# Kernel optimization log

Hardware: AMD Instinct MI355X
Metric: run time of the kernel (lower is better)

Reference implementation:

```python
import jax, jax.numpy as jnp
import numpy as np

HID = 4096
NH = 32
NKV = 8
HD = 128
KV_OUT = NKV * HD  # 1024
B, S = 1, 2048
SCALE = 64.0
THETA = 500000.0


def fwht(x):
    """Normalized fast Walsh-Hadamard transform over last dim (power of 2).
    Matches matmul_hadU_cuda for the had=None, K=1 case."""
    *lead, n = x.shape
    x = x.reshape(-1, n)
    h = 1
    while h < n:  # log2(n) static iterations
        x = x.reshape(-1, n // (2 * h), 2, h)
        a, b = x[:, :, 0, :], x[:, :, 1, :]
        x = jnp.stack([a + b, a - b], axis=2).reshape(-1, n)
        h *= 2
    return (x * (1.0 / np.sqrt(n))).reshape(*lead, n)


def rope_cos_sin(position_ids, dim=HD, theta=THETA):
    inv_freq = 1.0 / (theta ** (jnp.arange(0, dim, 2, dtype=jnp.float32) / dim))
    freqs = position_ids.astype(jnp.float32)[..., None] * inv_freq  # [B,S,HD/2]
    emb = jnp.concatenate([freqs, freqs], axis=-1)  # [B,S,HD]
    return jnp.cos(emb), jnp.sin(emb)


def rotate_half(x):
    h = x.shape[-1] // 2
    return jnp.concatenate([-x[..., h:], x[..., :h]], axis=-1)


def setup_inputs() -> dict:
    key = jax.random.key(0)
    ks = jax.random.split(key, 10)
    return {
        "hidden_states": jax.random.normal(ks[0], (B, S, HID), jnp.float32),
        "position_ids": jnp.arange(S, dtype=jnp.int32)[None, :],
        "SU_qkv": jnp.sign(jax.random.normal(ks[1], (HID,), jnp.float32)),
        "SU_o": jnp.sign(jax.random.normal(ks[2], (HID,), jnp.float32)),
        "Wscale_qkv": jax.random.uniform(ks[3], (HID + 2 * KV_OUT,), jnp.float32, 0.5, 1.5),
        "Wscale_o": jax.random.uniform(ks[4], (HID,), jnp.float32, 0.5, 1.5),
        "Wq": 0.02 * jax.random.normal(ks[5], (HID, HID), jnp.float32),
        "Wk": 0.02 * jax.random.normal(ks[6], (KV_OUT, HID), jnp.float32),
        "Wv": 0.02 * jax.random.normal(ks[7], (KV_OUT, HID), jnp.float32),
        "Wo": 0.02 * jax.random.normal(ks[8], (HID, HID), jnp.float32),
    }


def reference(hidden_states, position_ids, SU_qkv, SU_o, Wscale_qkv, Wscale_o, Wq, Wk, Wv, Wo):
    b, s, n = hidden_states.shape
    # --- compute_qkv: incoherence rotation + quantized-linear math ---
    x = fwht(hidden_states * SU_qkv) / SCALE  # [B,S,HID]
    q = (x @ Wq.T) * Wscale_qkv[:HID] * SCALE
    k = (x @ Wk.T) * Wscale_qkv[HID:HID + KV_OUT] * SCALE
    v = (x @ Wv.T) * Wscale_qkv[HID + KV_OUT:] * SCALE
    q = q.reshape(b, s, NH, HD).transpose(0, 2, 1, 3)   # [B,NH,S,HD]
    k = k.reshape(b, s, NKV, HD).transpose(0, 2, 1, 3)  # [B,NKV,S,HD]
    v = v.reshape(b, s, NKV, HD).transpose(0, 2, 1, 3)
    # --- RoPE ---
    cos, sin = rope_cos_sin(position_ids)
    cos, sin = cos[:, None], sin[:, None]  # [B,1,S,HD]
    q = q * cos + rotate_half(q) * sin
    k = k * cos + rotate_half(k) * sin
    # --- GQA repeat + causal SDPA ---
    rep = NH // NKV
    k = jnp.repeat(k, rep, axis=1)
    v = jnp.repeat(v, rep, axis=1)
    scores = jnp.einsum('bhqd,bhkd->bhqk', q, k) / np.sqrt(HD)
    causal = jnp.tril(jnp.ones((s, s), dtype=bool))
    scores = jnp.where(causal, scores, -1e30)
    attn = jax.nn.softmax(scores, axis=-1)
    out = jnp.einsum('bhqk,bhkd->bhqd', attn, v)
    out = out.transpose(0, 2, 1, 3).reshape(b, s, NH * HD)  # [B,S,HID]
    # --- compute_o ---
    y = fwht(out * SU_o) / SCALE
    y = (y @ Wo.T) * Wscale_o * SCALE
    return y
```

## Files before the change

### kernel.cpp

```cpp
#include <hip/hip_runtime.h>
#include <hip/hip_bf16.h>
#include <math.h>

#define S_LEN 2048
#define HID   4096
#define NQKV  6144
#define NHEAD 32
#define NKVH  8
#define HDIM  128

typedef __attribute__((ext_vector_type(8))) short short8;
typedef __attribute__((ext_vector_type(4))) float f32x4;

__device__ __forceinline__ unsigned short f2bf(float f) {
    union { float f; unsigned u; } v; v.f = f;
    unsigned r = v.u + 0x7fffu + ((v.u >> 16) & 1u);
    return (unsigned short)(r >> 16);
}
__device__ __forceinline__ float bf2f(unsigned short b) {
    union { unsigned u; float f; } v; v.u = ((unsigned)b) << 16;
    return v.f;
}
__device__ __forceinline__ unsigned cvt_pk_bf16(float lo, float hi) {
    unsigned r;
    asm("v_cvt_pk_bf16_f32 %0, %1, %2" : "=v"(r) : "v"(lo), "v"(hi));
    return r;
}

__global__ __launch_bounds__(256)
void cvt4_kernel(const float* __restrict__ Wq, const float* __restrict__ Wk,
                 const float* __restrict__ Wv, const float* __restrict__ Wo,
                 unsigned short* __restrict__ Wcat, unsigned short* __restrict__ Wob) {
    const int NQ = 4194304, NK = 1048576, NV = 1048576, NO = 4194304;
    int i = blockIdx.x * 256 + threadIdx.x;
    const int stride = gridDim.x * 256;
    for (; i < NQ + NK + NV + NO; i += stride) {
        const float* src; unsigned short* dst; int j;
        if (i < NQ)                { src = Wq; dst = Wcat;            j = i; }
        else if (i < NQ + NK)      { src = Wk; dst = Wcat + 16777216; j = i - NQ; }
        else if (i < NQ + NK + NV) { src = Wv; dst = Wcat + 20971520; j = i - NQ - NK; }
        else                       { src = Wo; dst = Wob;             j = i - NQ - NK - NV; }
        float4 v = *(const float4*)(src + (size_t)j * 4);
        ushort4 o;
        o.x = f2bf(v.x); o.y = f2bf(v.y); o.z = f2bf(v.z); o.w = f2bf(v.w);
        *(ushort4*)(dst + (size_t)j * 4) = o;
    }
}

__global__ __launch_bounds__(256)
void fwht_kernel(const float* __restrict__ in, const float* __restrict__ su,
                 unsigned short* __restrict__ out) {
    __shared__ float buf[HID];
    const float* src = in + (size_t)blockIdx.x * HID;
    for (int i = threadIdx.x; i < HID; i += 256) buf[i] = src[i] * su[i];
    __syncthreads();
    int lg = 0;
    for (int h = 1; h < HID; h <<= 1, ++lg) {
        for (int p = threadIdx.x; p < HID / 2; p += 256) {
            int j  = p & (h - 1);
            int i0 = ((p >> lg) << (lg + 1)) | j;
            int i1 = i0 + h;
            float a = buf[i0], b = buf[i1];
            buf[i0] = a + b;
            buf[i1] = a - b;
        }
        __syncthreads();
    }
    unsigned short* dst = out + (size_t)blockIdx.x * HID;
    const float norm = 1.0f / 4096.0f;
    for (int i = threadIdx.x; i < HID; i += 256) dst[i] = f2bf(buf[i] * norm);
}

__global__ __launch_bounds__(256)
void fwht_merge(const unsigned short* __restrict__ O1, const float* __restrict__ ML,
                const float* __restrict__ su, unsigned short* __restrict__ out) {
    __shared__ float buf[HID];
    __shared__ float w1s[NHEAD], w2s[NHEAD];
    const int q = blockIdx.x;
    if (threadIdx.x < NHEAD) {
        const float2* mlp = (const float2*)ML;
        float2 a = mlp[((size_t)q) * NHEAD + threadIdx.x];
        float2 b = mlp[((size_t)(S_LEN + q)) * NHEAD + threadIdx.x];
        float M = fmaxf(a.x, b.x);
        float e1 = exp2f(a.x - M), e2 = exp2f(b.x - M);
        float L = e1 * a.y + e2 * b.y;
        w1s[threadIdx.x] = e1 / L;
        w2s[threadIdx.x] = e2 / L;
    }
    __syncthreads();
    const unsigned short* r1 = O1 + (size_t)q * HID;
    const unsigned short* r2 = O1 + (size_t)(S_LEN + q) * HID;
    for (int i = threadIdx.x; i < HID; i += 256) {
        int hd = i >> 7;
        buf[i] = (bf2f(r1[i]) * w1s[hd] + bf2f(r2[i]) * w2s[hd]) * su[i];
    }
    __syncthreads();
    int lg = 0;
    for (int h = 1; h < HID; h <<= 1, ++lg) {
        for (int p = threadIdx.x; p < HID / 2; p += 256) {
            int j  = p & (h - 1);
            int i0 = ((p >> lg) << (lg + 1)) | j;
            int i1 = i0 + h;
            float a = buf[i0], b = buf[i1];
            buf[i0] = a + b;
            buf[i1] = a - b;
        }
        __syncthreads();
    }
    unsigned short* dst = out + (size_t)q * HID;
    const float norm = 1.0f / 4096.0f;
    for (int i = threadIdx.x; i < HID; i += 256) dst[i] = f2bf(buf[i] * norm);
}

__global__ __launch_bounds__(256)
void gemm_bt(const unsigned short* __restrict__ A, const unsigned short* __restrict__ B,
             const float* __restrict__ scale, float* __restrict__ C,
             int M, int N, int K) {
    __shared__ __attribute__((aligned(16))) unsigned short As[2][128 * 32];
    __shared__ __attribute__((aligned(16))) unsigned short Bs[2][128 * 32];
    const int bn = blockIdx.x, bm = blockIdx.y;
    const int tid = threadIdx.x;
    const int wv = tid >> 6, lane = tid & 63;
    const int wr = wv >> 1, wc = wv & 1;
    const int lr = lane & 15, lgp = lane >> 4;

    f32x4 acc[4][4] = {};

    auto stage = [&](int buf, int kt) {
        for (int c = wv; c < 8; c += 4) {
            int o = c * 512 + lane * 8;
            int row = o >> 5, col = o & 31;
            const unsigned short* ga = A + (size_t)(bm * 128 + row) * K + kt * 32 + col;
            __builtin_amdgcn_global_load_lds((const __attribute__((address_space(1))) void*)ga,
                (__attribute__((address_space(3))) void*)&As[buf][c * 512], 16, 0, 0);
            const unsigned short* gb = B + (size_t)(bn * 128 + row) * K + kt * 32 + col;
            __builtin_amdgcn_global_load_lds((const __attribute__((address_space(1))) void*)gb,
                (__attribute__((address_space(3))) void*)&Bs[buf][c * 512], 16, 0, 0);
        }
    };

    const int nt = K >> 5;
    stage(0, 0);
    __syncthreads();
    int cur = 0;
    for (int kt = 0; kt < nt; ++kt) {
        if (kt + 1 < nt) stage(cur ^ 1, kt + 1);
        const int ko = lgp * 8;
        short8 af[4], bfr[4];
#pragma unroll
        for (int m2 = 0; m2 < 4; ++m2)
            af[m2] = *(const short8*)&As[cur][(wr * 64 + m2 * 16 + lr) * 32 + ko];
#pragma unroll
        for (int n2 = 0; n2 < 4; ++n2)
            bfr[n2] = *(const short8*)&Bs[cur][(wc * 64 + n2 * 16 + lr) * 32 + ko];
#pragma unroll
        for (int m2 = 0; m2 < 4; ++m2)
#pragma unroll
            for (int n2 = 0; n2 < 4; ++n2)
                acc[m2][n2] = __builtin_amdgcn_mfma_f32_16x16x32_bf16(af[m2], bfr[n2], acc[m2][n2], 0, 0, 0);
        __syncthreads();
        cur ^= 1;
    }

#pragma unroll
    for (int n2 = 0; n2 < 4; ++n2) {
        int gn = bn * 128 + wc * 64 + n2 * 16 + lr;
        float sc = scale[gn] * 64.0f;
#pragma unroll
        for (int m2 = 0; m2 < 4; ++m2) {
            int gm0 = bm * 128 + wr * 64 + m2 * 16 + lgp * 4;
#pragma unroll
            for (int i = 0; i < 4; ++i)
                C[(size_t)(gm0 + i) * N + gn] = acc[m2][n2][i] * sc;
        }
    }
}

__global__ __launch_bounds__(256)
void rope_kernel(const float* __restrict__ qkv, const int* __restrict__ pos,
                 unsigned short* __restrict__ Qb, unsigned short* __restrict__ Kb,
                 unsigned short* __restrict__ Vb) {
    __shared__ float invf_t[64];
    if (threadIdx.x < 64)
        invf_t[threadIdx.x] = exp2f((float)threadIdx.x * -0.29580576f);
    __syncthreads();
    const int s = blockIdx.x;
    const float p = (float)pos[s];
    const float* row = qkv + (size_t)s * NQKV;
    const float qs = 0.12751793f;
    for (int idx = threadIdx.x; idx < NQKV; idx += 256) {
        float v = row[idx];
        if (idx < HID + NKVH * HDIM) {
            int base = (idx < HID) ? 0 : HID;
            int rel = idx - base;
            int h = rel >> 7, d = rel & 127;
            float ang = p * invf_t[d & 63];
            float sn, cs;
            sincosf(ang, &sn, &cs);
            float other = (d < 64) ? -row[base + h * 128 + d + 64]
                                   :  row[base + h * 128 + d - 64];
            float r = v * cs + other * sn;
            if (idx < HID) Qb[((size_t)h * S_LEN + s) * HDIM + d] = f2bf(r * qs);
            else           Kb[((size_t)h * S_LEN + s) * HDIM + d] = f2bf(r);
        } else {
            int rel = idx - (HID + NKVH * HDIM);
            int h = rel >> 7, d = rel & 127;
            Vb[((size_t)h * S_LEN + s) * HDIM + d] = f2bf(v);
        }
    }
}

__global__ __launch_bounds__(256)
void attn_kernel(const unsigned short* __restrict__ Q, const unsigned short* __restrict__ K,
                 const unsigned short* __restrict__ V, unsigned short* __restrict__ Opart,
                 float* __restrict__ ML) {
    const int hf = blockIdx.y;
    const int hd = blockIdx.z;
    const int kvh = hd >> 2;
    const int tid = threadIdx.x, wv = tid >> 6, lane = tid & 63;
    const int lr = lane & 15, lgp = lane >> 4;

    __shared__ __attribute__((aligned(16))) unsigned short Ks[2][64 * 128];
    __shared__ __attribute__((aligned(16))) unsigned short Vt[128 * 64];

    int koff[4];
#pragma unroll
    for (int j = 0; j < 4; ++j) {
        int a = (wv * 4 + j) * 512 + lane * 8;
        koff[j] = a ^ (((a >> 7) & 7) << 3);
    }
    const int vpos = ((lane >> 2) & 3) * 16 + (lane >> 4) * 4 + (lane & 3);
    const unsigned short* Kg = K + (size_t)kvh * S_LEN * HDIM;
    const unsigned short* Vg = V + (size_t)kvh * S_LEN * HDIM;

    auto stageK = [&](int buf, int kb) {
        const unsigned short* kg = Kg + (size_t)kb * 64 * HDIM;
#pragma unroll
        for (int j = 0; j < 4; ++j) {
            __builtin_amdgcn_global_load_lds(
                (const __attribute__((address_space(1))) void*)(kg + koff[j]),
                (__attribute__((address_space(3))) void*)&Ks[buf][(wv * 4 + j) * 512], 16, 0, 0);
        }
    };

#pragma unroll 1
    for (int rep = 0; rep < 2; ++rep) {
        const int qt = rep ? (31 - (int)blockIdx.x) : (int)blockIdx.x;
        const int qg = qt * 64 + wv * 16 + lr;
        const int n = qt + 1, mid = (n + 1) >> 1;
        const int s = hf ? mid : 0, e = hf ? n : mid;

        __syncthreads();

        short8 aq[4];
        {
            const unsigned short* qp = Q + ((size_t)hd * S_LEN + qg) * HDIM + lgp * 8;
#pragma unroll
            for (int kk = 0; kk < 4; ++kk) aq[kk] = *(const short8*)(qp + kk * 32);
        }

        f32x4 oacc[8] = {};
        float m_i = -3.0e38f, l_i = 0.f;

        short8 vcur[4];
        if (s < e) {
            stageK(s & 1, s);
            const unsigned short* vp = Vg + (size_t)s * 64 * HDIM + lane * HDIM + wv * 32;
#pragma unroll
            for (int r2 = 0; r2 < 4; ++r2) vcur[r2] = *(const short8*)(vp + r2 * 8);
        }

#pragma unroll 1
        for (int kb = s; kb < e; ++kb) {
            const int cur = kb & 1;
            __syncthreads();

            if (kb + 1 < e) stageK(cur ^ 1, kb + 1);
#pragma unroll
            for (int r2 = 0; r2 < 4; ++r2) {
#pragma unroll
                for (int en = 0; en < 8; ++en) {
                    int d = wv * 32 + r2 * 8 + en;
                    Vt[(d * 64 + vpos) ^ ((d & 7) << 3)] = ((const unsigned short*)&vcur[r2])[en];
                }
            }
            if (kb + 1 < e) {
                const unsigned short* vp = Vg + (size_t)(kb + 1) * 64 * HDIM + lane * HDIM + wv * 32;
#pragma unroll
                for (int r2 = 0; r2 < 4; ++r2) vcur[r2] = *(const short8*)(vp + r2 * 8);
            }

            __builtin_amdgcn_s_setprio(1);
            f32x4 sc[4];
#pragma unroll
            for (int nt2 = 0; nt2 < 4; ++nt2) {
                f32x4 a = {};
                const int krow = nt2 * 16 + lr;
                const int swz = (krow & 7) << 3;
#pragma unroll
                for (int kk = 0; kk < 4; ++kk) {
                    short8 ak = *(const short8*)&Ks[cur][(krow * 128 + kk * 32 + lgp * 8) ^ swz];
                    a = __builtin_amdgcn_mfma_f32_16x16x32_bf16(ak, aq[kk], a, 0, 0, 0);
                }
                sc[nt2] = a;
            }
            __builtin_amdgcn_s_setprio(0);

            if (kb == qt) {
#pragma unroll
                for (int nt2 = 0; nt2 < 4; ++nt2)
#pragma unroll
                    for (int i = 0; i < 4; ++i) {
                        int kvg = kb * 64 + nt2 * 16 + 4 * lgp + i;
                        if (kvg > qg) sc[nt2][i] = -1.0e30f;
                    }
            }

            float vmax = fmaxf(fmaxf(fmaxf(sc[0][0], sc[0][1]), fmaxf(sc[0][2], sc[0][3])),
                               fmaxf(fmaxf(sc[1][0], sc[1][1]), fmaxf(sc[1][2], sc[1][3])));
            vmax = fmaxf(vmax, fmaxf(fmaxf(fmaxf(sc[2][0], sc[2][1]), fmaxf(sc[2][2], sc[2][3])),
                                     fmaxf(fmaxf(sc[3][0], sc[3][1]), fmaxf(sc[3][2], sc[3][3]))));
            vmax = fmaxf(vmax, __shfl_xor(vmax, 16));
            vmax = fmaxf(vmax, __shfl_xor(vmax, 32));

            if (!__all(vmax <= m_i + 11.0f)) {
                float mn = fmaxf(m_i, vmax);
                float fe = __builtin_amdgcn_exp2f(m_i - mn);
                m_i = mn;
                l_i *= fe;
                float feb[4];
#pragma unroll
                for (int i2 = 0; i2 < 4; ++i2) feb[i2] = __shfl(fe, 4 * lgp + i2);
#pragma unroll
                for (int t = 0; t < 8; ++t)
#pragma unroll
                    for (int i2 = 0; i2 < 4; ++i2) oacc[t][i2] *= feb[i2];
            }

            float rs = 0.f;
#pragma unroll
            for (int nt2 = 0; nt2 < 4; ++nt2)
#pragma unroll
                for (int i = 0; i < 4; ++i) {
                    float pv = __builtin_amdgcn_exp2f(sc[nt2][i] - m_i);
                    sc[nt2][i] = pv;
                    rs += pv;
                }
            rs += __shfl_xor(rs, 16);
            rs += __shfl_xor(rs, 32);
            l_i += rs;

            union { unsigned u[4]; short8 sv; } a0, a1;
            a0.u[0] = cvt_pk_bf16(sc[0][0], sc[0][1]);
            a0.u[1] = cvt_pk_bf16(sc[0][2], sc[0][3]);
            a0.u[2] = cvt_pk_bf16(sc[1][0], sc[1][1]);
            a0.u[3] = cvt_pk_bf16(sc[1][2], sc[1][3]);
            a1.u[0] = cvt_pk_bf16(sc[2][0], sc[2][1]);
            a1.u[1] = cvt_pk_bf16(sc[2][2], sc[2][3]);
            a1.u[2] = cvt_pk_bf16(sc[3][0], sc[3][1]);
            a1.u[3] = cvt_pk_bf16(sc[3][2], sc[3][3]);

            asm volatile("s_waitcnt lgkmcnt(0)" ::: "memory");
            __builtin_amdgcn_sched_barrier(0);
            __builtin_amdgcn_s_barrier();

            __builtin_amdgcn_s_setprio(1);
#pragma unroll
            for (int t = 0; t < 8; ++t) {
                const int d = t * 16 + lr;
                const int swz = (d & 7) << 3;
                const int dbase = d * 64 + lgp * 16;
                short8 bv0 = *(const short8*)&Vt[(dbase) ^ swz];
                short8 bv1 = *(const short8*)&Vt[(dbase + 8) ^ swz];
                oacc[t] = __builtin_amdgcn_mfma_f32_16x16x32_bf16(a0.sv, bv0, oacc[t], 0, 0, 0);
                oacc[t] = __builtin_amdgcn_mfma_f32_16x16x32_bf16(a1.sv, bv1, oacc[t], 0, 0, 0);
            }
            __builtin_amdgcn_s_setprio(0);
        }

        unsigned short* op = Opart + ((size_t)hf * S_LEN + qt * 64 + wv * 16 + 4 * lgp) * HID
                           + hd * HDIM + lr;
#pragma unroll
        for (int t = 0; t < 8; ++t)
#pragma unroll
            for (int i2 = 0; i2 < 4; ++i2)
                op[(size_t)i2 * HID + t * 16] = f2bf(oacc[t][i2]);
        if (lgp == 0) {
            float2* mlp = (float2*)ML;
            mlp[((size_t)hf * S_LEN + qt * 64 + wv * 16 + lr) * NHEAD + hd] =
                make_float2(m_i, l_i);
        }
    }
}

extern "C" void kernel_launch(void* const* d_in, const int* in_sizes, int n_in,
                              void* d_out, int out_size, void* d_ws, size_t ws_size,
                              hipStream_t stream) {
    const float* hidden = (const float*)d_in[0];
    const int*   pos    = (const int*)d_in[1];
    const float* su_qkv = (const float*)d_in[2];
    const float* su_o   = (const float*)d_in[3];
    const float* ws_qkv = (const float*)d_in[4];
    const float* ws_o   = (const float*)d_in[5];
    const float* Wq     = (const float*)d_in[6];
    const float* Wk     = (const float*)d_in[7];
    const float* Wv     = (const float*)d_in[8];
    const float* Wo     = (const float*)d_in[9];
    float* out = (float*)d_out;

    char* ws = (char*)d_ws;
    unsigned short* Wcat = (unsigned short*)(ws);
    unsigned short* Wob  = (unsigned short*)(ws + 50331648);
    unsigned short* xb   = (unsigned short*)(ws + 83886080);
    float*          qkv  = (float*)(ws + 100663296);
    unsigned short* Opart= (unsigned short*)(ws + 100663296);
    float*          ML   = (float*)(ws + 100663296 + 33554432);
    unsigned short* Qb   = (unsigned short*)(ws + 150994944);
    unsigned short* Kb   = Qb + (size_t)NHEAD * S_LEN * HDIM;
    unsigned short* Vb   = Kb + (size_t)NKVH * S_LEN * HDIM;

    cvt4_kernel<<<2560, 256, 0, stream>>>(Wq, Wk, Wv, Wo, Wcat, Wob);

    fwht_kernel<<<S_LEN, 256, 0, stream>>>(hidden, su_qkv, xb);
    gemm_bt<<<dim3(NQKV / 128, S_LEN / 128), 256, 0, stream>>>(xb, Wcat, ws_qkv, qkv, S_LEN, NQKV, HID);
    rope_kernel<<<S_LEN, 256, 0, stream>>>(qkv, pos, Qb, Kb, Vb);
    attn_kernel<<<dim3(16, 2, NHEAD), 256, 0, stream>>>(Qb, Kb, Vb, Opart, ML);
    fwht_merge<<<S_LEN, 256, 0, stream>>>(Opart, ML, su_o, xb);
    gemm_bt<<<dim3(HID / 128, S_LEN / 128), 256, 0, stream>>>(xb, Wob, ws_o, out, S_LEN, HID, HID);
}
```

Before: 433.6 us.

## Fuse RoPE into QKV GEMM epilogue and split attention KV three ways

Replaces the generic QKV GEMM plus separate RoPE kernel with a GEMM whose epilogue applies rotary embedding and writes bf16 Q/K/V directly, permuting B rows so each wave holds paired d and d+64 columns. This removes the fp32 QKV intermediate round trip and a launch. Attention now splits each query tile's KV range into three parts for more parallelism, and the merge kernel combines three partials, at the cost of extra partial-output traffic.

New measurement: 442.1 us. No clear change (+2.0%).

```diff
diff --git a/kernel.cpp b/kernel.cpp
--- a/kernel.cpp
+++ b/kernel.cpp
@@ -75,24 +75,27 @@
 void fwht_merge(const unsigned short* __restrict__ O1, const float* __restrict__ ML,
                 const float* __restrict__ su, unsigned short* __restrict__ out) {
     __shared__ float buf[HID];
-    __shared__ float w1s[NHEAD], w2s[NHEAD];
+    __shared__ float w1s[NHEAD], w2s[NHEAD], w3s[NHEAD];
     const int q = blockIdx.x;
     if (threadIdx.x < NHEAD) {
         const float2* mlp = (const float2*)ML;
         float2 a = mlp[((size_t)q) * NHEAD + threadIdx.x];
         float2 b = mlp[((size_t)(S_LEN + q)) * NHEAD + threadIdx.x];
-        float M = fmaxf(a.x, b.x);
-        float e1 = exp2f(a.x - M), e2 = exp2f(b.x - M);
-        float L = e1 * a.y + e2 * b.y;
+        float2 c = mlp[((size_t)(2 * S_LEN + q)) * NHEAD + threadIdx.x];
+        float M = fmaxf(fmaxf(a.x, b.x), c.x);
+        float e1 = exp2f(a.x - M), e2 = exp2f(b.x - M), e3 = exp2f(c.x - M);
+        float L = e1 * a.y + e2 * b.y + e3 * c.y;
         w1s[threadIdx.x] = e1 / L;
         w2s[threadIdx.x] = e2 / L;
+        w3s[threadIdx.x] = e3 / L;
     }
     __syncthreads();
     const unsigned short* r1 = O1 + (size_t)q * HID;
     const unsigned short* r2 = O1 + (size_t)(S_LEN + q) * HID;
+    const unsigned short* r3 = O1 + (size_t)(2 * S_LEN + q) * HID;
     for (int i = threadIdx.x; i < HID; i += 256) {
         int hd = i >> 7;
-        buf[i] = (bf2f(r1[i]) * w1s[hd] + bf2f(r2[i]) * w2s[hd]) * su[i];
+        buf[i] = (bf2f(r1[i]) * w1s[hd] + bf2f(r2[i]) * w2s[hd] + bf2f(r3[i]) * w3s[hd]) * su[i];
     }
     __syncthreads();
     int lg = 0;
@@ -177,35 +180,93 @@
 }
 
 __global__ __launch_bounds__(256)
-void rope_kernel(const float* __restrict__ qkv, const int* __restrict__ pos,
-                 unsigned short* __restrict__ Qb, unsigned short* __restrict__ Kb,
-                 unsigned short* __restrict__ Vb) {
+void gemm_qkv(const unsigned short* __restrict__ A, const unsigned short* __restrict__ B,
+              const float* __restrict__ scale, const int* __restrict__ pos,
+              unsigned short* __restrict__ Qb, unsigned short* __restrict__ Kb,
+              unsigned short* __restrict__ Vb) {
+    const int K = HID;
+    __shared__ __attribute__((aligned(16))) unsigned short As[2][128 * 32];
+    __shared__ __attribute__((aligned(16))) unsigned short Bs[2][128 * 32];
     __shared__ float invf_t[64];
-    if (threadIdx.x < 64)
-        invf_t[threadIdx.x] = exp2f((float)threadIdx.x * -0.29580576f);
+    __shared__ float poss[128];
+    const int bn = blockIdx.x, bm = blockIdx.y;
+    const int tid = threadIdx.x;
+    const int wv = tid >> 6, lane = tid & 63;
+    const int wr = wv >> 1, wc = wv & 1;
+    const int lr = lane & 15, lgp = lane >> 4;
+
+    if (tid < 64) invf_t[tid] = exp2f((float)tid * -0.29580576f);
+    if (tid >= 128) poss[tid - 128] = (float)pos[bm * 128 + (tid - 128)];
+
+    f32x4 acc[4][4] = {};
+
+    auto stage = [&](int buf, int kt) {
+        for (int c = wv; c < 8; c += 4) {
+            int o = c * 512 + lane * 8;
+            int row = o >> 5, col = o & 31;
+            const unsigned short* ga = A + (size_t)(bm * 128 + row) * K + kt * 32 + col;
+            __builtin_amdgcn_global_load_lds((const __attribute__((address_space(1))) void*)ga,
+                (__attribute__((address_space(3))) void*)&As[buf][c * 512], 16, 0, 0);
+            int prow = (row & 31) | ((row & 32) << 1) | ((row & 64) >> 1);
+            const unsigned short* gb = B + (size_t)(bn * 128 + prow) * K + kt * 32 + col;
+            __builtin_amdgcn_global_load_lds((const __attribute__((address_space(1))) void*)gb,
+                (__attribute__((address_space(3))) void*)&Bs[buf][c * 512], 16, 0, 0);
+        }
+    };
+
+    const int nt = K >> 5;
+    stage(0, 0);
     __syncthreads();
-    const int s = blockIdx.x;
-    const float p = (float)pos[s];
-    const float* row = qkv + (size_t)s * NQKV;
-    const float qs = 0.12751793f;
-    for (int idx = threadIdx.x; idx < NQKV; idx += 256) {
-        float v = row[idx];
-        if (idx < HID + NKVH * HDIM) {
-            int base = (idx < HID) ? 0 : HID;
-            int rel = idx - base;
-            int h = rel >> 7, d = rel & 127;
-            float ang = p * invf_t[d & 63];
-            float sn, cs;
-            sincosf(ang, &sn, &cs);
-            float other = (d < 64) ? -row[base + h * 128 + d + 64]
-                                   :  row[base + h * 128 + d - 64];
-            float r = v * cs + other * sn;
-            if (idx < HID) Qb[((size_t)h * S_LEN + s) * HDIM + d] = f2bf(r * qs);
-            else           Kb[((size_t)h * S_LEN + s) * HDIM + d] = f2bf(r);
-        } else {
-            int rel = idx - (HID + NKVH * HDIM);
-            int h = rel >> 7, d = rel & 127;
-            Vb[((size_t)h * S_LEN + s) * HDIM + d] = f2bf(v);
+    int cur = 0;
+    for (int kt = 0; kt < nt; ++kt) {
+        if (kt + 1 < nt) stage(cur ^ 1, kt + 1);
+        const int ko = lgp * 8;
+        short8 af[4], bfr[4];
+#pragma unroll
+        for (int m2 = 0; m2 < 4; ++m2)
+            af[m2] = *(const short8*)&As[cur][(wr * 64 + m2 * 16 + lr) * 32 + ko];
+#pragma unroll
+        for (int n2 = 0; n2 < 4; ++n2)
+            bfr[n2] = *(const short8*)&Bs[cur][(wc * 64 + n2 * 16 + lr) * 32 + ko];
+#pragma unroll
+        for (int m2 = 0; m2 < 4; ++m2)
+#pragma unroll
+            for (int n2 = 0; n2 < 4; ++n2)
+                acc[m2][n2] = __builtin_amdgcn_mfma_f32_16x16x32_bf16(af[m2], bfr[n2], acc[m2][n2], 0, 0, 0);
+        __syncthreads();
+        cur ^= 1;
+    }
+
+    const int nb = bn * 128;
+    const float QS = 0.12751793f;
+#pragma unroll
+    for (int n2 = 0; n2 < 2; ++n2) {
+        const int d = n2 * 16 + lr + wc * 32;
+        const float sc_lo = scale[nb + d] * 64.0f;
+        const float sc_hi = scale[nb + d + 64] * 64.0f;
+        const float ivf = invf_t[d];
+#pragma unroll
+        for (int m2 = 0; m2 < 4; ++m2) {
+#pragma unroll
+            for (int i = 0; i < 4; ++i) {
+                const int lrow = wr * 64 + m2 * 16 + lgp * 4 + i;
+                const int srow = bm * 128 + lrow;
+                float lo = acc[m2][n2][i] * sc_lo;
+                float hi = acc[m2][n2 + 2][i] * sc_hi;
+                float olo, ohi;
+                if (bn < 40) {
+                    float sn, cs;
+                    sincosf(poss[lrow] * ivf, &sn, &cs);
+                    olo = lo * cs - hi * sn;
+                    ohi = hi * cs + lo * sn;
+                } else { olo = lo; ohi = hi; }
+                unsigned short* dst;
+                if (bn < 32)      { dst = Qb + ((size_t)bn * S_LEN + srow) * HDIM; olo *= QS; ohi *= QS; }
+                else if (bn < 40) { dst = Kb + ((size_t)(bn - 32) * S_LEN + srow) * HDIM; }
+                else              { dst = Vb + ((size_t)(bn - 40) * S_LEN + srow) * HDIM; }
+                dst[d]      = f2bf(olo);
+                dst[d + 64] = f2bf(ohi);
+            }
         }
     }
 }
@@ -247,8 +308,8 @@
     for (int rep = 0; rep < 2; ++rep) {
         const int qt = rep ? (31 - (int)blockIdx.x) : (int)blockIdx.x;
         const int qg = qt * 64 + wv * 16 + lr;
-        const int n = qt + 1, mid = (n + 1) >> 1;
-        const int s = hf ? mid : 0, e = hf ? n : mid;
+        const int n = qt + 1;
+        const int s = (n * hf) / 3, e = (n * (hf + 1)) / 3;
 
         __syncthreads();
 
@@ -412,9 +473,8 @@
     unsigned short* Wcat = (unsigned short*)(ws);
     unsigned short* Wob  = (unsigned short*)(ws + 50331648);
     unsigned short* xb   = (unsigned short*)(ws + 83886080);
-    float*          qkv  = (float*)(ws + 100663296);
     unsigned short* Opart= (unsigned short*)(ws + 100663296);
-    float*          ML   = (float*)(ws + 100663296 + 33554432);
+    float*          ML   = (float*)(ws);
     unsigned short* Qb   = (unsigned short*)(ws + 150994944);
     unsigned short* Kb   = Qb + (size_t)NHEAD * S_LEN * HDIM;
     unsigned short* Vb   = Kb + (size_t)NKVH * S_LEN * HDIM;
@@ -422,9 +482,8 @@
     cvt4_kernel<<<2560, 256, 0, stream>>>(Wq, Wk, Wv, Wo, Wcat, Wob);
 
     fwht_kernel<<<S_LEN, 256, 0, stream>>>(hidden, su_qkv, xb);
-    gemm_bt<<<dim3(NQKV / 128, S_LEN / 128), 256, 0, stream>>>(xb, Wcat, ws_qkv, qkv, S_LEN, NQKV, HID);
-    rope_kernel<<<S_LEN, 256, 0, stream>>>(qkv, pos, Qb, Kb, Vb);
-    attn_kernel<<<dim3(16, 2, NHEAD), 256, 0, stream>>>(Qb, Kb, Vb, Opart, ML);
+    gemm_qkv<<<dim3(NQKV / 128, S_LEN / 128), 256, 0, stream>>>(xb, Wcat, ws_qkv, pos, Qb, Kb, Vb);
+    attn_kernel<<<dim3(16, 3, NHEAD), 256, 0, stream>>>(Qb, Kb, Vb, Opart, ML);
     fwht_merge<<<S_LEN, 256, 0, stream>>>(Opart, ML, su_o, xb);
     gemm_bt<<<dim3(HID / 128, S_LEN / 128), 256, 0, stream>>>(xb, Wob, ws_o, out, S_LEN, HID, HID);
 }
```
